# Performance work log

Measured on AMD Instinct MI355X. Metric: run time of the kernel, lower is better.

The kernel has to match this reference:

```python
import jax, jax.numpy as jnp
import numpy as np

N = 50000
E = 800000
G = 64
H, C = 16, 4  # heads, out_channels per head; H*C = 64


def setup_inputs() -> dict:
    key = jax.random.key(0)
    ks = jax.random.split(key, 16)
    return {
        "x": jax.random.normal(ks[0], (N,), jnp.float32),
        "edge_index": jax.random.randint(ks[1], (2, E), 0, N),
        "edge_attr": jax.random.normal(ks[2], (E,), jnp.float32),
        "batch": jnp.sort(jax.random.randint(ks[3], (N,), 0, G)),
        # GATv2Conv(1 -> 4, heads=16, edge_dim=1, concat=True)
        "Wl": jax.random.normal(ks[4], (1, H * C), jnp.float32) * 0.5,
        "bl": jnp.full((H * C,), 0.01, jnp.float32),
        "Wr": jax.random.normal(ks[5], (1, H * C), jnp.float32) * 0.5,
        "br": jnp.full((H * C,), 0.01, jnp.float32),
        "We": jax.random.normal(ks[6], (1, H * C), jnp.float32) * 0.5,
        "att": jax.random.normal(ks[7], (H, C), jnp.float32) * 0.5,
        "gat_bias": jnp.zeros((H * C,), jnp.float32),
        # GraphNorm(64)
        "gn_w": jnp.ones((H * C,), jnp.float32),
        "gn_b": jnp.zeros((H * C,), jnp.float32),
        "gn_ms": jnp.ones((H * C,), jnp.float32),
        # SAGEConv(64 -> 64, mean aggr, root weight)
        "sage_Wl": jax.random.normal(ks[8], (H * C, 64), jnp.float32) * 0.125,
        "sage_bl": jnp.full((64,), 0.01, jnp.float32),
        "sage_Wr": jax.random.normal(ks[9], (H * C, 64), jnp.float32) * 0.125,
        # MLP head
        "fc1_W": jax.random.normal(ks[10], (128, 2048), jnp.float32) * 0.08,
        "fc1_b": jnp.full((2048,), 0.01, jnp.float32),
        "fc2_W": jax.random.normal(ks[11], (2048, 1024), jnp.float32) * 0.02,
        "fc2_b": jnp.full((1024,), 0.01, jnp.float32),
        "fc3_W": jax.random.normal(ks[12], (1024, 3), jnp.float32) * 0.03,
        "fc3_b": jnp.full((3,), 0.01, jnp.float32),
    }


def reference(x, edge_index, edge_attr, batch, Wl, bl, Wr, br, We, att, gat_bias,
              gn_w, gn_b, gn_ms, sage_Wl, sage_bl, sage_Wr,
              fc1_W, fc1_b, fc2_W, fc2_b, fc3_W, fc3_b):
    src0, dst0 = edge_index[0], edge_index[1]
    x1 = x[:, None]  # [N,1] (torch.unsqueeze(x, -1))
    # ---- GATv2Conv ----
    xl = (x1 @ Wl + bl).reshape(N, H, C)  # source-side (x_j, also the value)
    xr = (x1 @ Wr + br).reshape(N, H, C)  # target-side (x_i)
    # add self loops; fill_value='mean' -> per-node mean of incoming edge_attr
    deg_in = jax.ops.segment_sum(jnp.ones((E,), x.dtype), dst0, num_segments=N)
    loop_attr = jax.ops.segment_sum(edge_attr, dst0, num_segments=N) / jnp.maximum(deg_in, 1.0)
    loops = jnp.arange(N)
    src = jnp.concatenate([src0, loops])
    dst = jnp.concatenate([dst0, loops])
    ea = jnp.concatenate([edge_attr, loop_attr])[:, None]  # [E+N,1]
    e = (ea @ We).reshape(-1, H, C)
    m = jax.nn.leaky_relu(xl[src] + xr[dst] + e, 0.2)  # [E+N,H,C]
    score = jnp.einsum('ehc,hc->eh', m, att)
    smax = jax.ops.segment_max(score, dst, num_segments=N)
    a = jnp.exp(score - smax[dst])
    denom = jax.ops.segment_sum(a, dst, num_segments=N)
    alpha = a / denom[dst]  # segmented softmax over incoming edges
    h = jax.ops.segment_sum(alpha[:, :, None] * xl[src], dst, num_segments=N)
    h = h.reshape(N, H * C) + gat_bias
    h = jax.nn.relu(h)
    # ---- GraphNorm ----
    cnt = jax.ops.segment_sum(jnp.ones((N,), x.dtype), batch, num_segments=G)[:, None]
    mean = jax.ops.segment_sum(h, batch, num_segments=G) / cnt
    o = h - mean[batch] * gn_ms
    var = jax.ops.segment_sum(o * o, batch, num_segments=G) / cnt
    h = gn_w * o / jnp.sqrt(var[batch] + 1e-5) + gn_b
    # ---- SAGEConv (mean aggregation + root weight) ----
    neigh = jax.ops.segment_sum(h[src0], dst0, num_segments=N) / jnp.maximum(deg_in, 1.0)[:, None]
    h = neigh @ sage_Wl + sage_bl + h @ sage_Wr
    h = jax.nn.relu(h)
    # ---- global max + mean pooling, MLP head (eval mode: dropout off) ----
    gmax = jax.ops.segment_max(h, batch, num_segments=G)
    gmean = jax.ops.segment_sum(h, batch, num_segments=G) / cnt
    g = jnp.concatenate([gmax, gmean], axis=1)  # [G, 128]
    g = jax.nn.relu(g @ fc1_W + fc1_b)
    g = jax.nn.relu(g @ fc2_W + fc2_b)
    return g @ fc3_W + fc3_b
```

## Files before the change

kernel.cpp:

```cpp
#include <hip/hip_runtime.h>

#define GG 64
#define HH 16
#define KK 64
#define S_SUB 8

__device__ __forceinline__ float bf2f(unsigned short u){
  return __uint_as_float(((unsigned)u) << 16);
}
__device__ __forceinline__ unsigned short f2bf(float f){
  unsigned u = __float_as_uint(f);
  unsigned r = u + 0x7fffu + ((u >> 16) & 1u);
  return (unsigned short)(r >> 16);
}


__global__ void k_count_rank(const int* __restrict__ ei, int* deg, int* __restrict__ rank, int E){
  int e = blockIdx.x*blockDim.x + threadIdx.x;
  if (e < E) rank[e] = atomicAdd(&deg[ei[E + e]], 1);
}

__global__ void k_scan1(const int* __restrict__ deg, int* __restrict__ bsum, int N){
  int base = blockIdx.x*1024;
  int lim = min(base + 1024, N);
  int s = 0;
  for (int i = base + (int)threadIdx.x; i < lim; i += 256) s += deg[i];
  #pragma unroll
  for (int ofs = 32; ofs >= 1; ofs >>= 1) s += __shfl_down(s, ofs, 64);
  __shared__ int ws[4];
  int lane = threadIdx.x & 63, wv = threadIdx.x >> 6;
  if (lane == 0) ws[wv] = s;
  __syncthreads();
  if (threadIdx.x == 0) bsum[blockIdx.x] = ws[0] + ws[1] + ws[2] + ws[3];
}

__global__ void __launch_bounds__(1024)
k_scan2(int* __restrict__ bsum, int* __restrict__ row_start_N, int NB){
  int t = threadIdx.x;
  int v = (t < NB) ? bsum[t] : 0;
  int lane = t & 63, wv = t >> 6;
  int val = v;
  #pragma unroll
  for (int ofs = 1; ofs < 64; ofs <<= 1){
    int tt = __shfl_up(val, ofs, 64);
    if (lane >= ofs) val += tt;
  }
  __shared__ int ws[16];
  if (lane == 63) ws[wv] = val;
  __syncthreads();
  if (t == 0){
    int run = 0;
    #pragma unroll
    for (int w = 0; w < 16; ++w){ int tmp = ws[w]; ws[w] = run; run += tmp; }
  }
  __syncthreads();
  int excl = ws[wv] + val - v;
  if (t < NB) bsum[t] = excl;
  if (t == NB - 1) *row_start_N = excl + v;
}

__global__ void k_scan3(const int* __restrict__ deg, const int* __restrict__ bsum,
                        int* __restrict__ row_start, int N){
  int b = blockIdx.x;
  int base = b*1024 + (int)threadIdx.x*4;
  int d0 = (base+0 < N) ? deg[base+0] : 0;
  int d1 = (base+1 < N) ? deg[base+1] : 0;
  int d2 = (base+2 < N) ? deg[base+2] : 0;
  int d3 = (base+3 < N) ? deg[base+3] : 0;
  int s = d0 + d1 + d2 + d3;
  int lane = threadIdx.x & 63, wv = threadIdx.x >> 6;
  int val = s;
  #pragma unroll
  for (int ofs = 1; ofs < 64; ofs <<= 1){
    int tt = __shfl_up(val, ofs, 64);
    if (lane >= ofs) val += tt;
  }
  __shared__ int ws[4];
  if (lane == 63) ws[wv] = val;
  __syncthreads();
  if (threadIdx.x == 0){
    int run = 0;
    #pragma unroll
    for (int w = 0; w < 4; ++w){ int tmp = ws[w]; ws[w] = run; run += tmp; }
  }
  __syncthreads();
  int pre = bsum[b] + ws[wv] + val - s;
  if (base+0 < N){ row_start[base+0] = pre; pre += d0; }
  if (base+1 < N){ row_start[base+1] = pre; pre += d1; }
  if (base+2 < N){ row_start[base+2] = pre; pre += d2; }
  if (base+3 < N){ row_start[base+3] = pre; }
}

__global__ void k_scatter(const int* __restrict__ ei, const float* __restrict__ ea,
                          const int* __restrict__ row_start, const int* __restrict__ rank,
                          int2* __restrict__ csr_se, int E){
  int e = blockIdx.x*blockDim.x + threadIdx.x;
  if (e >= E) return;
  int d = ei[E + e];
  int pos = row_start[d] + rank[e];
  csr_se[pos] = make_int2(ei[e], __float_as_int(ea[e]));
}

__global__ void k_gbounds(const int* __restrict__ batch, int N, int* __restrict__ goff){
  int g = threadIdx.x;
  if (g > GG) return;
  int lo = 0, hi = N;
  while (lo < hi){ int mid = (lo+hi) >> 1; if (batch[mid] < g) lo = mid+1; else hi = mid; }
  goff[g] = lo;
}

__global__ void k_gat(const float* __restrict__ x, const int* __restrict__ row_start,
                      const int2* __restrict__ cse,
                      const float* __restrict__ Wl, const float* __restrict__ bl,
                      const float* __restrict__ Wr, const float* __restrict__ br,
                      const float* __restrict__ We, const float* __restrict__ att,
                      const float* __restrict__ gat_bias,
                      float* __restrict__ h, int N){
  int t = blockIdx.x*blockDim.x + threadIdx.x;
  int n   = t >> 2;
  int sub = t & 3;
  if (n >= N) return;
  float xd = x[n];
  float wl[16], we[16], at[16], pre[16];
  int k0 = sub*16;
  #pragma unroll
  for (int i = 0; i < 16; ++i){
    int k = k0 + i;
    wl[i] = Wl[k]; we[i] = We[k]; at[i] = att[k];
    pre[i] = bl[k] + fmaf(xd, Wr[k], br[k]);
  }
  int e0 = row_start[n], e1 = row_start[n+1];
  float m[4]  = {-3.4e38f,-3.4e38f,-3.4e38f,-3.4e38f};
  float den[4] = {0,0,0,0}, S1[4] = {0,0,0,0};
  float asum = 0.f;

#define PROC(XS, EAV)                                                        \
  { float xs_ = (XS), ea_ = (EAV);                                           \
    _Pragma("unroll")                                                        \
    for (int hi2 = 0; hi2 < 4; ++hi2){                                       \
      float sc = 0.f;                                                        \
      _Pragma("unroll")                                                      \
      for (int c = 0; c < 4; ++c){                                           \
        int i = hi2*4 + c;                                                   \
        float tt = fmaf(xs_, wl[i], fmaf(ea_, we[i], pre[i]));               \
        tt = (tt > 0.f) ? tt : 0.2f*tt;                                      \
        sc = fmaf(tt, at[i], sc);                                            \
      }                                                                      \
      float nm = fmaxf(m[hi2], sc);                                          \
      float corr = __expf(m[hi2] - nm);                                      \
      float a    = __expf(sc - nm);                                          \
      den[hi2] = den[hi2]*corr + a;                                          \
      S1[hi2]  = S1[hi2] *corr + a*xs_;                                      \
      m[hi2] = nm; } }

  int e = e0;
  for (; e + 3 < e1; e += 4){
    int2 p0 = cse[e], p1 = cse[e+1], p2 = cse[e+2], p3 = cse[e+3];
    float xs0 = x[p0.x], xs1 = x[p1.x], xs2 = x[p2.x], xs3 = x[p3.x];
    float ea0 = __int_as_float(p0.y), ea1 = __int_as_float(p1.y);
    float ea2 = __int_as_float(p2.y), ea3 = __int_as_float(p3.y);
    asum += (ea0 + ea1) + (ea2 + ea3);
    PROC(xs0, ea0);
    PROC(xs1, ea1);
    PROC(xs2, ea2);
    PROC(xs3, ea3);
  }
  for (; e < e1; ++e){
    int2 p0 = cse[e];
    float xs0 = x[p0.x], ea0 = __int_as_float(p0.y);
    asum += ea0;
    PROC(xs0, ea0);
  }
  {
    float degf = (float)(e1 - e0);
    float eav = asum / fmaxf(degf, 1.0f);
    PROC(xd, eav);
  }
#undef PROC
  #pragma unroll
  for (int hi2 = 0; hi2 < 4; ++hi2){
    float r = S1[hi2] / den[hi2];
    float4 o;
    #pragma unroll
    for (int c = 0; c < 4; ++c){
      int i = hi2*4 + c, k = k0 + i;
      float v = fmaxf(fmaf(wl[i], r, bl[k] + gat_bias[k]), 0.f);
      ((float*)&o)[c] = v;
    }
    *(float4*)(h + (size_t)n*KK + k0 + hi2*4) = o;
  }
}

__global__ void k_gstats_part(const float* __restrict__ h, const int* __restrict__ goff,
                              float* __restrict__ gsum, float* __restrict__ gsum2){
  int g = blockIdx.x, sb = blockIdx.y;
  int s = goff[g], epos = goff[g+1];
  int k = threadIdx.x & 63, slice = threadIdx.x >> 6;
  float sum = 0.f, sum2 = 0.f;
  for (int n = s + sb*4 + slice; n < epos; n += S_SUB*4){
    float v = h[(size_t)n*KK + k];
    sum += v; sum2 += v*v;
  }
  __shared__ float ls[4][KK], ls2[4][KK];
  ls[slice][k] = sum; ls2[slice][k] = sum2;
  __syncthreads();
  if (slice == 0){
    float a  = ls[0][k]+ls[1][k]+ls[2][k]+ls[3][k];
    float b2 = ls2[0][k]+ls2[1][k]+ls2[2][k]+ls2[3][k];
    atomicAdd(&gsum[g*KK + k], a);
    atomicAdd(&gsum2[g*KK + k], b2);
  }
}

__global__ void k_norm(float* __restrict__ h, unsigned short* __restrict__ hb,
                       const int* __restrict__ batch,
                       const float* __restrict__ gsum, const float* __restrict__ gsum2,
                       const int* __restrict__ goff,
                       const float* __restrict__ gn_w, const float* __restrict__ gn_b,
                       const float* __restrict__ gn_ms, int N){
  int t = blockIdx.x*blockDim.x + threadIdx.x;
  if (t >= N*16) return;
  int n = t >> 4, q = t & 15;
  int b = batch[n];
  float c = fmaxf((float)(goff[b+1] - goff[b]), 1.0f);
  float inv = 1.0f / c;
  float4 hv = *(float4*)(h + (size_t)n*KK + q*4);
  float ov[4];
  #pragma unroll
  for (int i = 0; i < 4; ++i){
    int k = q*4 + i;
    float mean = gsum[b*KK + k]*inv;
    float eh2  = gsum2[b*KK + k]*inv;
    float ms = gn_ms[k];
    float var = eh2 - 2.f*ms*mean*mean + ms*ms*mean*mean;
    float sc = gn_w[k] * __frsqrt_rn(var + 1e-5f);
    float sh = gn_b[k] - sc*mean*ms;
    ov[i] = fmaf(sc, ((float*)&hv)[i], sh);
  }
  *(float4*)(h + (size_t)n*KK + q*4) = make_float4(ov[0], ov[1], ov[2], ov[3]);
  ushort4 bv;
  bv.x = f2bf(ov[0]); bv.y = f2bf(ov[1]); bv.z = f2bf(ov[2]); bv.w = f2bf(ov[3]);
  *(ushort4*)(hb + (size_t)n*KK + q*4) = bv;
}

__global__ void k_sage(const float* __restrict__ h, const unsigned short* __restrict__ hb,
                       const int* __restrict__ row_start, const int2* __restrict__ cse,
                       const float* __restrict__ Wl, const float* __restrict__ bln,
                       const float* __restrict__ Wr,
                       float* __restrict__ h2, int N){
  __shared__ float snm[16][KK], shn[16][KK];
  const ushort4* hb4 = (const ushort4*)hb;
  int tid = threadIdx.x;
  int u = tid >> 4;
  int q = tid & 15;
  int n = blockIdx.x*16 + u;
  if (n < N){
    int e0 = row_start[n], e1 = row_start[n+1];
    float a0=0.f,a1=0.f,a2=0.f,a3=0.f;
    float b0=0.f,b1=0.f,b2=0.f,b3=0.f;
    int e = e0;
    for (; e + 7 < e1; e += 8){
      int s0 = cse[e].x,   s1 = cse[e+1].x, s2 = cse[e+2].x, s3 = cse[e+3].x;
      int s4 = cse[e+4].x, s5 = cse[e+5].x, s6 = cse[e+6].x, s7 = cse[e+7].x;
      ushort4 v0 = hb4[(size_t)s0*16 + q];
      ushort4 v1 = hb4[(size_t)s1*16 + q];
      ushort4 v2 = hb4[(size_t)s2*16 + q];
      ushort4 v3 = hb4[(size_t)s3*16 + q];
      ushort4 v4 = hb4[(size_t)s4*16 + q];
      ushort4 v5 = hb4[(size_t)s5*16 + q];
      ushort4 v6 = hb4[(size_t)s6*16 + q];
      ushort4 v7 = hb4[(size_t)s7*16 + q];
      a0 += bf2f(v0.x); a1 += bf2f(v0.y); a2 += bf2f(v0.z); a3 += bf2f(v0.w);
      b0 += bf2f(v1.x); b1 += bf2f(v1.y); b2 += bf2f(v1.z); b3 += bf2f(v1.w);
      a0 += bf2f(v2.x); a1 += bf2f(v2.y); a2 += bf2f(v2.z); a3 += bf2f(v2.w);
      b0 += bf2f(v3.x); b1 += bf2f(v3.y); b2 += bf2f(v3.z); b3 += bf2f(v3.w);
      a0 += bf2f(v4.x); a1 += bf2f(v4.y); a2 += bf2f(v4.z); a3 += bf2f(v4.w);
      b0 += bf2f(v5.x); b1 += bf2f(v5.y); b2 += bf2f(v5.z); b3 += bf2f(v5.w);
      a0 += bf2f(v6.x); a1 += bf2f(v6.y); a2 += bf2f(v6.z); a3 += bf2f(v6.w);
      b0 += bf2f(v7.x); b1 += bf2f(v7.y); b2 += bf2f(v7.z); b3 += bf2f(v7.w);
    }
    for (; e < e1; ++e){
      ushort4 v0 = hb4[(size_t)cse[e].x*16 + q];
      a0 += bf2f(v0.x); a1 += bf2f(v0.y); a2 += bf2f(v0.z); a3 += bf2f(v0.w);
    }
    float dg = fmaxf((float)(e1 - e0), 1.0f);
    float inv = 1.0f/dg;
    float4 nm = make_float4((a0+b0)*inv, (a1+b1)*inv, (a2+b2)*inv, (a3+b3)*inv);
    *(float4*)&snm[u][q*4] = nm;
    *(float4*)&shn[u][q*4] = *(const float4*)(h + (size_t)n*KK + q*4);
  }
  __syncthreads();
  int j = tid & 63, u0 = tid >> 6;
  float acc[4];
  #pragma unroll
  for (int p = 0; p < 4; ++p) acc[p] = bln[j];
  for (int k = 0; k < KK; ++k){
    float wlv = Wl[k*KK + j], wrv = Wr[k*KK + j];
    #pragma unroll
    for (int p = 0; p < 4; ++p){
      int un = u0 + p*4;
      acc[p] = fmaf(snm[un][k], wlv, acc[p]);
      acc[p] = fmaf(shn[un][k], wrv, acc[p]);
    }
  }
  #pragma unroll
  for (int p = 0; p < 4; ++p){
    int un = u0 + p*4;
    int nn = blockIdx.x*16 + un;
    if (nn < N) h2[(size_t)nn*KK + j] = fmaxf(acc[p], 0.f);
  }
}

__global__ void k_pool_part(const float* __restrict__ h2, const int* __restrict__ goff,
                            unsigned* __restrict__ gmaxu, float* __restrict__ gsumP){
  int g = blockIdx.x, sb = blockIdx.y;
  int s = goff[g], epos = goff[g+1];
  int k = threadIdx.x & 63, slice = threadIdx.x >> 6;
  float mx = 0.f, sm = 0.f;
  for (int n = s + sb*4 + slice; n < epos; n += S_SUB*4){
    float v = h2[(size_t)n*KK + k];
    mx = fmaxf(mx, v); sm += v;
  }
  __shared__ float lm[4][KK], lsum[4][KK];
  lm[slice][k] = mx; lsum[slice][k] = sm;
  __syncthreads();
  if (slice == 0){
    float m2 = fmaxf(fmaxf(lm[0][k], lm[1][k]), fmaxf(lm[2][k], lm[3][k]));
    float s2 = lsum[0][k]+lsum[1][k]+lsum[2][k]+lsum[3][k];
    atomicMax(&gmaxu[g*KK + k], __float_as_uint(m2));
    atomicAdd(&gsumP[g*KK + k], s2);
  }
}


__global__ void k_fc1(const unsigned* __restrict__ gmaxu, const float* __restrict__ gsumP,
                      const int* __restrict__ goff,
                      const float* __restrict__ W, const float* __restrict__ b,
                      float* __restrict__ out){
  __shared__ float sin[128];
  int g = blockIdx.y, jt = blockIdx.x;
  int tid = threadIdx.x;
  if (tid < 128){
    float c = fmaxf((float)(goff[g+1] - goff[g]), 1.0f);
    sin[tid] = (tid < 64) ? __uint_as_float(gmaxu[g*64 + tid])
                          : gsumP[g*64 + (tid-64)] / c;
  }
  __syncthreads();
  int j = jt*256 + tid;
  float acc = b[j];
  #pragma unroll 16
  for (int k = 0; k < 128; ++k)
    acc = fmaf(sin[k], W[(size_t)k*2048 + j], acc);
  out[(size_t)g*2048 + j] = fmaxf(acc, 0.f);
}

__global__ void k_fc2a(const float* __restrict__ in, const float* __restrict__ W,
                       float* __restrict__ partial){
  __shared__ float sin[64][128];
  int jt = blockIdx.x, ks = blockIdx.y;
  int k0 = ks*128;
  int tid = threadIdx.x;
  for (int idx = tid; idx < 64*128; idx += 256){
    int g = idx >> 7, k = idx & 127;
    sin[g][k] = in[(size_t)g*2048 + k0 + k];
  }
  __syncthreads();
  int j = tid & 63, gs = tid >> 6;
  const float* Wp = W + (size_t)k0*1024 + jt*64 + j;
  float acc[16];
  #pragma unroll
  for (int p = 0; p < 16; ++p) acc[p] = 0.f;
  for (int k = 0; k < 128; ++k){
    float w = Wp[(size_t)k*1024];
    #pragma unroll
    for (int p = 0; p < 16; ++p)
      acc[p] = fmaf(sin[gs*16 + p][k], w, acc[p]);
  }
  #pragma unroll
  for (int p = 0; p < 16; ++p){
    int g = gs*16 + p;
    partial[((size_t)ks*64 + g)*1024 + jt*64 + j] = acc[p];
  }
}

__global__ void k_fc2red(const float* __restrict__ partial, const float* __restrict__ b,
                         float* __restrict__ out){
  int i = blockIdx.x*blockDim.x + threadIdx.x;
  int g = i >> 10, j = i & 1023;
  float s = b[j];
  #pragma unroll
  for (int ks = 0; ks < 16; ++ks)
    s += partial[((size_t)ks*64 + g)*1024 + j];
  out[i] = fmaxf(s, 0.f);
}

__global__ void k_fc3(const float* __restrict__ in, const float* __restrict__ W,
                      const float* __restrict__ b, float* __restrict__ out, int nOut){
  int w = (blockIdx.x*blockDim.x + threadIdx.x) >> 6;
  int lane = threadIdx.x & 63;
  if (w >= GG*nOut) return;
  int g = w / nOut, j = w - g*nOut;
  const float* row = in + (size_t)g*1024;
  float acc = 0.f;
  #pragma unroll
  for (int k = lane; k < 1024; k += 64)
    acc = fmaf(row[k], W[(size_t)k*nOut + j], acc);
  #pragma unroll
  for (int ofs = 32; ofs >= 1; ofs >>= 1)
    acc += __shfl_down(acc, ofs, 64);
  if (lane == 0) out[w] = acc + b[j];
}

extern "C" void kernel_launch(void* const* d_in, const int* in_sizes, int n_in,
                              void* d_out, int out_size, void* d_ws, size_t ws_size,
                              hipStream_t stream) {
  const float* x        = (const float*)d_in[0];
  const int*   ei       = (const int*)d_in[1];
  const float* ea       = (const float*)d_in[2];
  const int*   batch    = (const int*)d_in[3];
  const float* Wl       = (const float*)d_in[4];
  const float* bl       = (const float*)d_in[5];
  const float* Wr       = (const float*)d_in[6];
  const float* br       = (const float*)d_in[7];
  const float* We       = (const float*)d_in[8];
  const float* att      = (const float*)d_in[9];
  const float* gat_bias = (const float*)d_in[10];
  const float* gn_w     = (const float*)d_in[11];
  const float* gn_b     = (const float*)d_in[12];
  const float* gn_ms    = (const float*)d_in[13];
  const float* sage_Wl  = (const float*)d_in[14];
  const float* sage_bl  = (const float*)d_in[15];
  const float* sage_Wr  = (const float*)d_in[16];
  const float* fc1_W    = (const float*)d_in[17];
  const float* fc1_b    = (const float*)d_in[18];
  const float* fc2_W    = (const float*)d_in[19];
  const float* fc2_b    = (const float*)d_in[20];
  const float* fc3_W    = (const float*)d_in[21];
  const float* fc3_b    = (const float*)d_in[22];

  const int N = in_sizes[0];
  const int E = in_sizes[1] / 2;
  const int NB = (N + 1023) / 1024;

  char* ws = (char*)d_ws;
  size_t off = 0;
  auto alloc = [&](size_t bytes){ void* p = ws + off; off += (bytes + 255) & ~(size_t)255; return p; };

  int*      deg_i  = (int*)alloc((size_t)N*4);
  float*    gsum   = (float*)alloc(GG*KK*4);
  float*    gsum2  = (float*)alloc(GG*KK*4);
  unsigned* gmaxu  = (unsigned*)alloc(GG*KK*4);
  float*    gsumP  = (float*)alloc(GG*KK*4);
  size_t zero_bytes = off;
  int*   rank      = (int*)alloc((size_t)E*4);
  int*   bsum      = (int*)alloc((size_t)NB*4);
  int*   row_start = (int*)alloc((size_t)(N+1)*4);
  int*   goff      = (int*)alloc((GG+1)*4);
  int2*  csr_se    = (int2*)alloc((size_t)E*8);
  float* h         = (float*)alloc((size_t)N*KK*4);
  unsigned short* hb = (unsigned short*)alloc((size_t)N*KK*2);
  float* h2        = (float*)alloc((size_t)N*KK*4);
  float* out1      = (float*)alloc((size_t)GG*2048*4);
  float* out2      = (float*)alloc((size_t)GG*1024*4);
  float* partial   = (float*)alloc((size_t)16*GG*1024*4);
  (void)ws_size; (void)n_in; (void)out_size;

  hipMemsetAsync(d_ws, 0, zero_bytes, stream);

  const int B = 256;
  k_count_rank<<<(E+B-1)/B, B, 0, stream>>>(ei, deg_i, rank, E);
  k_gbounds<<<1, 128, 0, stream>>>(batch, N, goff);
  k_scan1  <<<NB, B, 0, stream>>>(deg_i, bsum, N);
  k_scan2  <<<1, 1024, 0, stream>>>(bsum, row_start + N, NB);
  k_scan3  <<<NB, B, 0, stream>>>(deg_i, bsum, row_start, N);
  k_scatter<<<(E+B-1)/B, B, 0, stream>>>(ei, ea, row_start, rank, csr_se, E);
  k_gat    <<<((size_t)N*4+B-1)/B, B, 0, stream>>>(x, row_start, csr_se,
                                                   Wl, bl, Wr, br, We, att, gat_bias, h, N);
  {
    dim3 grid(GG, S_SUB);
    k_gstats_part<<<grid, 256, 0, stream>>>(h, goff, gsum, gsum2);
  }
  k_norm   <<<((size_t)N*16+B-1)/B, B, 0, stream>>>(h, hb, batch, gsum, gsum2, goff,
                                                    gn_w, gn_b, gn_ms, N);
  k_sage   <<<(N+15)/16, B, 0, stream>>>(h, hb, row_start, csr_se, sage_Wl, sage_bl, sage_Wr, h2, N);
  {
    dim3 grid(GG, S_SUB);
    k_pool_part<<<grid, 256, 0, stream>>>(h2, goff, gmaxu, gsumP);
  }
  {
    dim3 grid(8, GG);
    k_fc1  <<<grid, 256, 0, stream>>>(gmaxu, gsumP, goff, fc1_W, fc1_b, out1);
  }
  {
    dim3 grid(16, 16);
    k_fc2a <<<grid, 256, 0, stream>>>(out1, fc2_W, partial);
  }
  k_fc2red <<<(GG*1024+B-1)/B, B, 0, stream>>>(partial, fc2_b, out2);
  k_fc3    <<<(GG*3*64+B-1)/B, B, 0, stream>>>(out2, fc3_W, fc3_b, (float*)d_out, 3);
}
```

Baseline: 207.3 us.

## Fuse memset with group-bounds kernel, widen GAT threads per node, add SAGE 4-tail

```diff
diff --git a/kernel.cpp b/kernel.cpp
--- a/kernel.cpp
+++ b/kernel.cpp
@@ -12,6 +12,19 @@
   unsigned u = __float_as_uint(f);
   unsigned r = u + 0x7fffu + ((u >> 16) & 1u);
   return (unsigned short)(r >> 16);
+}
+
+__global__ void k_zero(int4* __restrict__ p, int nInt4,
+                       const int* __restrict__ batch, int N, int* __restrict__ goff){
+  int t = blockIdx.x*blockDim.x + threadIdx.x;
+  for (int i = t; i < nInt4; i += gridDim.x*blockDim.x)
+    p[i] = make_int4(0,0,0,0);
+  if (blockIdx.x == 0 && threadIdx.x <= GG){
+    int g = threadIdx.x;
+    int lo = 0, hi = N;
+    while (lo < hi){ int mid = (lo+hi) >> 1; if (batch[mid] < g) lo = mid+1; else hi = mid; }
+    goff[g] = lo;
+  }
 }
 
 
@@ -101,14 +114,6 @@
   csr_se[pos] = make_int2(ei[e], __float_as_int(ea[e]));
 }
 
-__global__ void k_gbounds(const int* __restrict__ batch, int N, int* __restrict__ goff){
-  int g = threadIdx.x;
-  if (g > GG) return;
-  int lo = 0, hi = N;
-  while (lo < hi){ int mid = (lo+hi) >> 1; if (batch[mid] < g) lo = mid+1; else hi = mid; }
-  goff[g] = lo;
-}
-
 __global__ void k_gat(const float* __restrict__ x, const int* __restrict__ row_start,
                       const int2* __restrict__ cse,
                       const float* __restrict__ Wl, const float* __restrict__ bl,
@@ -117,27 +122,27 @@
                       const float* __restrict__ gat_bias,
                       float* __restrict__ h, int N){
   int t = blockIdx.x*blockDim.x + threadIdx.x;
-  int n   = t >> 2;
-  int sub = t & 3;
+  int n   = t >> 3;
+  int sub = t & 7;
   if (n >= N) return;
   float xd = x[n];
-  float wl[16], we[16], at[16], pre[16];
-  int k0 = sub*16;
-  #pragma unroll
-  for (int i = 0; i < 16; ++i){
+  float wl[8], we[8], at[8], pre[8];
+  int k0 = sub*8;
+  #pragma unroll
+  for (int i = 0; i < 8; ++i){
     int k = k0 + i;
     wl[i] = Wl[k]; we[i] = We[k]; at[i] = att[k];
     pre[i] = bl[k] + fmaf(xd, Wr[k], br[k]);
   }
   int e0 = row_start[n], e1 = row_start[n+1];
-  float m[4]  = {-3.4e38f,-3.4e38f,-3.4e38f,-3.4e38f};
-  float den[4] = {0,0,0,0}, S1[4] = {0,0,0,0};
+  float m[2]  = {-3.4e38f,-3.4e38f};
+  float den[2] = {0,0}, S1[2] = {0,0};
   float asum = 0.f;
 
 #define PROC(XS, EAV)                                                        \
   { float xs_ = (XS), ea_ = (EAV);                                           \
     _Pragma("unroll")                                                        \
-    for (int hi2 = 0; hi2 < 4; ++hi2){                                       \
+    for (int hi2 = 0; hi2 < 2; ++hi2){                                       \
       float sc = 0.f;                                                        \
       _Pragma("unroll")                                                      \
       for (int c = 0; c < 4; ++c){                                           \
@@ -178,7 +183,7 @@
   }
 #undef PROC
   #pragma unroll
-  for (int hi2 = 0; hi2 < 4; ++hi2){
+  for (int hi2 = 0; hi2 < 2; ++hi2){
     float r = S1[hi2] / den[hi2];
     float4 o;
     #pragma unroll
@@ -279,6 +284,18 @@
       a0 += bf2f(v6.x); a1 += bf2f(v6.y); a2 += bf2f(v6.z); a3 += bf2f(v6.w);
       b0 += bf2f(v7.x); b1 += bf2f(v7.y); b2 += bf2f(v7.z); b3 += bf2f(v7.w);
     }
+    if (e + 3 < e1){
+      int s0 = cse[e].x, s1 = cse[e+1].x, s2 = cse[e+2].x, s3 = cse[e+3].x;
+      ushort4 v0 = hb4[(size_t)s0*16 + q];
+      ushort4 v1 = hb4[(size_t)s1*16 + q];
+      ushort4 v2 = hb4[(size_t)s2*16 + q];
+      ushort4 v3 = hb4[(size_t)s3*16 + q];
+      a0 += bf2f(v0.x); a1 += bf2f(v0.y); a2 += bf2f(v0.z); a3 += bf2f(v0.w);
+      b0 += bf2f(v1.x); b1 += bf2f(v1.y); b2 += bf2f(v1.z); b3 += bf2f(v1.w);
+      a0 += bf2f(v2.x); a1 += bf2f(v2.y); a2 += bf2f(v2.z); a3 += bf2f(v2.w);
+      b0 += bf2f(v3.x); b1 += bf2f(v3.y); b2 += bf2f(v3.z); b3 += bf2f(v3.w);
+      e += 4;
+    }
     for (; e < e1; ++e){
       ushort4 v0 = hb4[(size_t)cse[e].x*16 + q];
       a0 += bf2f(v0.x); a1 += bf2f(v0.y); a2 += bf2f(v0.z); a3 += bf2f(v0.w);
@@ -465,16 +482,18 @@
   float* partial   = (float*)alloc((size_t)16*GG*1024*4);
   (void)ws_size; (void)n_in; (void)out_size;
 
-  hipMemsetAsync(d_ws, 0, zero_bytes, stream);
-
   const int B = 256;
+  {
+    int nInt4 = (int)(zero_bytes >> 4);
+    int blocks = min((nInt4 + B - 1)/B, 256);
+    k_zero <<<blocks, B, 0, stream>>>((int4*)d_ws, nInt4, batch, N, goff);
+  }
   k_count_rank<<<(E+B-1)/B, B, 0, stream>>>(ei, deg_i, rank, E);
-  k_gbounds<<<1, 128, 0, stream>>>(batch, N, goff);
   k_scan1  <<<NB, B, 0, stream>>>(deg_i, bsum, N);
   k_scan2  <<<1, 1024, 0, stream>>>(bsum, row_start + N, NB);
   k_scan3  <<<NB, B, 0, stream>>>(deg_i, bsum, row_start, N);
   k_scatter<<<(E+B-1)/B, B, 0, stream>>>(ei, ea, row_start, rank, csr_se, E);
-  k_gat    <<<((size_t)N*4+B-1)/B, B, 0, stream>>>(x, row_start, csr_se,
+  k_gat    <<<((size_t)N*8+B-1)/B, B, 0, stream>>>(x, row_start, csr_se,
                                                    Wl, bl, Wr, br, We, att, gat_bias, h, N);
   {
     dim3 grid(GG, S_SUB);
```

Result: faster. 191.7 us (-7.5%).
